# Optimization experiments

Measured on AMD Instinct MI355X. Metric: run time of the kernel, lower is better.

## Reference

```python
import jax, jax.numpy as jnp
import numpy as np

B, T, C = 2, 2048, 1024
H, D = 16, 64  # n_head, head_size = C // H


def setup_inputs() -> dict:
    key = jax.random.key(0)
    ks = jax.random.split(key, 6)
    s = 1.0 / np.sqrt(C)
    x = jax.random.normal(ks[0], (B, T, C), dtype=jnp.float32)
    Wq = jax.random.normal(ks[1], (C, C), dtype=jnp.float32) * s
    Wk = jax.random.normal(ks[2], (C, C), dtype=jnp.float32) * s
    Wv = jax.random.normal(ks[3], (C, C), dtype=jnp.float32) * s
    Wp = jax.random.normal(ks[4], (C, C), dtype=jnp.float32) * s
    bp = jnp.zeros((C,), dtype=jnp.float32)
    return {"x": x, "Wq": Wq, "Wk": Wk, "Wv": Wv, "Wp": Wp, "bp": bp}


def _feature_map(x):
    # F.elu(x) + 1.0
    return jnp.where(x > 0, x + 1.0, jnp.exp(x))


def reference(x, Wq, Wk, Wv, Wp, bp):
    Bx, Tx, Cx = x.shape
    # q,k,v projections (nn.Linear with weight W applies x @ W.T)
    q = (x @ Wq.T).reshape(Bx, Tx, H, D).transpose(0, 2, 1, 3)  # bhtd
    k = (x @ Wk.T).reshape(Bx, Tx, H, D).transpose(0, 2, 1, 3)
    v = (x @ Wv.T).reshape(Bx, Tx, H, D).transpose(0, 2, 1, 3)
    qp = _feature_map(q)
    kp = _feature_map(k)
    # cumulative outer-product context: (B,H,T,D,D)
    kv_cum = jnp.cumsum(jnp.einsum('bhsd,bhsv->bhsdv', kp, v), axis=2)
    ksum_cum = jnp.cumsum(kp, axis=2)  # (B,H,T,D)
    num = jnp.einsum('bhsd,bhsdv->bhsv', qp, kv_cum)
    den = jnp.einsum('bhsd,bhsd->bhs', qp, ksum_cum)[..., None] + 1e-6
    y = (num / den).transpose(0, 2, 1, 3).reshape(Bx, Tx, Cx)
    out = y @ Wp.T + bp  # dropout(p=0) is identity
    new_kv = kv_cum[:, :, -1]
    new_ksum = ksum_cum[:, :, -1]
    return (out, new_kv, new_ksum)
```

## Files before the change

kernel.cpp:

```cpp
#include <hip/hip_runtime.h>
#include <math.h>

#define BB 2
#define TT 2048
#define CC 1024
#define HH 16
#define DD 64
#define MM (BB*TT)
#define LCH 128
#define NCH (TT/LCH)
#define BHH (BB*HH)

#define OUT_OFF_KV   4194304
#define OUT_OFF_KSUM 4325376
#define MB 1048576

typedef unsigned int u32;
typedef unsigned short u16;
typedef __attribute__((ext_vector_type(8))) short s16x8;
typedef __attribute__((ext_vector_type(8))) unsigned short us8;
typedef __attribute__((ext_vector_type(4))) float f32x4;

__device__ __forceinline__ float fmap(float x) {
    return x > 0.0f ? x + 1.0f : expf(x);
}
__device__ __forceinline__ u16 bf16r(float f) {
    u32 u = __float_as_uint(f);
    u += 0x7fffu + ((u >> 16) & 1u);
    return (u16)(u >> 16);
}
__device__ __forceinline__ float bf2f(u16 u) {
    return __uint_as_float(((u32)u) << 16);
}
__device__ __forceinline__ void gload16(const void* g, void* l) {
    __builtin_amdgcn_global_load_lds(
        (const __attribute__((address_space(1))) u32*)g,
        (__attribute__((address_space(3))) u32*)l, 16, 0, 0);
}

__global__ __launch_bounds__(256)
void f2bf_all(const float* __restrict__ x,
              const float* __restrict__ Wq, const float* __restrict__ Wk,
              const float* __restrict__ Wv, const float* __restrict__ Wp,
              u16* __restrict__ xbf, u16* __restrict__ wbf)
{
    const int i = blockIdx.x * 256 + threadIdx.x;
    const float* src;
    u16* dst;
    int off;
    if (i < 524288) {
        src = x; dst = xbf; off = i;
    } else {
        const int j = i - 524288;
        const int sel = j >> 17;
        off = j & 131071;
        src = (sel == 0) ? Wq : (sel == 1) ? Wk : (sel == 2) ? Wv : Wp;
        dst = wbf + ((size_t)sel << 20);
    }
    const float4 a = ((const float4*)src)[off*2];
    const float4 b = ((const float4*)src)[off*2 + 1];
    us8 p;
    p[0]=bf16r(a.x); p[1]=bf16r(a.y); p[2]=bf16r(a.z); p[3]=bf16r(a.w);
    p[4]=bf16r(b.x); p[5]=bf16r(b.y); p[6]=bf16r(b.z); p[7]=bf16r(b.w);
    ((us8*)dst)[off] = p;
}

__global__ __launch_bounds__(512, 4)
void lca_gemm_qkv128(const u16* __restrict__ A, const u16* __restrict__ Wall,
                     u16* __restrict__ qp, u16* __restrict__ kp,
                     u16* __restrict__ kt, u16* __restrict__ vt)
{
    extern __shared__ char LB[];
    const int tid  = threadIdx.x;
    const int lane = tid & 63;
    const int wid  = tid >> 6;
    const int wm   = wid >> 2;
    const int wn   = wid & 3;
    const int bm0  = blockIdx.y * 128;
    const int bn0g = blockIdx.x * 128;
    const int sel  = bn0g >> 10;
    const int nn0  = bn0g & (CC-1);
    const u16* W = Wall + ((size_t)sel << 20);
    const int NT = CC / 64;

    const int srow = (wid << 3) + (lane >> 3);
    const int sg   = lane & 7;
    auto STAGE = [&](const u16* G, int ldsbase) {
        #pragma unroll
        for (int j = 0; j < 2; ++j) {
            const int r  = j*64 + srow;
            const int gs = sg ^ (r & 7);
            gload16(G + (size_t)r * CC + gs*8,
                    LB + ldsbase + (size_t)(j*64 + (wid<<3))*128);
        }
    };
    #define LDSA(slot) ((slot)*16384)
    #define LDSB(slot) (32768 + (slot)*16384)

    f32x4 acc[4][2];
    #pragma unroll
    for (int mi = 0; mi < 4; ++mi)
        #pragma unroll
        for (int ni = 0; ni < 2; ++ni)
            acc[mi][ni] = (f32x4){0.f, 0.f, 0.f, 0.f};

    STAGE(A + (size_t)bm0 * CC + 0, LDSA(0));
    STAGE(W + (size_t)nn0 * CC + 0, LDSB(0));

    const int lr  = lane & 15;
    const int lg4 = lane >> 4;

    for (int t = 0; t < NT; ++t) {
        const int slot = t & 1;

        if (t+1 < NT) {
            STAGE(A + (size_t)bm0 * CC + (t+1)*64, LDSA(slot^1));
            STAGE(W + (size_t)nn0 * CC + (t+1)*64, LDSB(slot^1));
        }
        __builtin_amdgcn_sched_barrier(0);
        if (t < NT-1) asm volatile("s_waitcnt vmcnt(4)" ::: "memory");
        else          asm volatile("s_waitcnt vmcnt(0)" ::: "memory");
        __builtin_amdgcn_s_barrier();

        s16x8 af[4][2], bf[2][2];
        #pragma unroll
        for (int mi = 0; mi < 4; ++mi) {
            const int r = wm*64 + mi*16 + lr;
            #pragma unroll
            for (int ks = 0; ks < 2; ++ks) {
                const int gg = (ks*4 + lg4) ^ (r & 7);
                af[mi][ks] = *(const s16x8*)(LB + LDSA(slot) + r*128 + gg*16);
            }
        }
        #pragma unroll
        for (int ni = 0; ni < 2; ++ni) {
            const int r = wn*32 + ni*16 + lr;
            #pragma unroll
            for (int ks = 0; ks < 2; ++ks) {
                const int gg = (ks*4 + lg4) ^ (r & 7);
                bf[ni][ks] = *(const s16x8*)(LB + LDSB(slot) + r*128 + gg*16);
            }
        }

        __builtin_amdgcn_s_setprio(1);
        #pragma unroll
        for (int mi = 0; mi < 4; ++mi)
            #pragma unroll
            for (int ni = 0; ni < 2; ++ni)
                #pragma unroll
                for (int ks = 0; ks < 2; ++ks)
                    acc[mi][ni] = __builtin_amdgcn_mfma_f32_16x16x32_bf16(
                        af[mi][ks], bf[ni][ks], acc[mi][ni], 0, 0, 0);
        __builtin_amdgcn_s_setprio(0);
        __builtin_amdgcn_sched_barrier(0);
        __builtin_amdgcn_s_barrier();
    }

    #pragma unroll
    for (int mi = 0; mi < 4; ++mi) {
        #pragma unroll
        for (int ni = 0; ni < 2; ++ni) {
            const int coln = nn0 + wn*32 + ni*16 + lr;
            const int rb   = bm0 + wm*64 + mi*16 + lg4*4;
            const int h = coln >> 6, d = coln & (DD-1);
            const int b = rb >> 11, t0 = rb & (TT-1);
            u16 bvv[4];
            #pragma unroll
            for (int r = 0; r < 4; ++r) {
                float val = acc[mi][ni][r];
                if (sel != 2) val = fmap(val);
                bvv[r] = bf16r(val);
            }
            if (sel == 0) {
                u16* p = qp + (((size_t)(b*HH + h)) * TT + t0) * DD + d;
                #pragma unroll
                for (int r = 0; r < 4; ++r) p[(size_t)r * DD] = bvv[r];
            } else {
                const int ch = t0 >> 7, tc = t0 & (LCH-1);
                u16* pt = (sel == 1 ? kt : vt)
                        + (((size_t)((b*HH + h)*NCH + ch)) * DD + d) * LCH + tc;
                *(ushort4*)pt = make_ushort4(bvv[0], bvv[1], bvv[2], bvv[3]);
                if (sel == 1) {
                    u16* p = kp + (((size_t)(b*HH + h)) * TT + t0) * DD + d;
                    #pragma unroll
                    for (int r = 0; r < 4; ++r) p[(size_t)r * DD] = bvv[r];
                }
            }
        }
    }
    #undef LDSA
    #undef LDSB
}

__global__ __launch_bounds__(256)
void lca_gemm_out(const u16* __restrict__ A, const u16* __restrict__ W,
                  const float* __restrict__ bias, float* __restrict__ out)
{
    __shared__ short As[2][4096];
    __shared__ short Bs2[2][2048];
    const int tid  = threadIdx.x;
    const int lane = tid & 63;
    const int wid  = tid >> 6;

    const int bid = blockIdx.y * gridDim.x + blockIdx.x;
    const int nb  = (bid & 7) * 64 + (bid >> 3);
    const int bm0 = (nb >> 4) * 128;
    const int bn0 = (nb & 15) * 64;

    const int wm = wid >> 1, wn = wid & 1;

    const int rsA = wid*32 + (lane >> 2);
    const int rsB = wid*16 + (lane >> 2);
    const int kc  = (lane & 3) * 8;

    f32x4 acc[4][2];
    #pragma unroll
    for (int i = 0; i < 4; ++i)
        #pragma unroll
        for (int j = 0; j < 2; ++j)
            acc[i][j] = (f32x4){0.f, 0.f, 0.f, 0.f};

    const int rA = wm*64 + (lane & 15);
    const int rB = wn*32 + (lane & 15);
    const int kk = (lane >> 4) * 8;

    #pragma unroll
    for (int j = 0; j < 2; ++j)
        gload16(A + (size_t)(bm0 + rsA + j*16) * CC + kc, &As[0][wid*1024 + j*512]);
    gload16(W + (size_t)(bn0 + rsB) * CC + kc, &Bs2[0][wid*512]);
    __syncthreads();

    int cur = 0;
    for (int k0 = 0; k0 < CC; k0 += 32) {
        if (k0 + 32 < CC) {
            #pragma unroll
            for (int j = 0; j < 2; ++j)
                gload16(A + (size_t)(bm0 + rsA + j*16) * CC + k0 + 32 + kc, &As[cur^1][wid*1024 + j*512]);
            gload16(W + (size_t)(bn0 + rsB) * CC + k0 + 32 + kc, &Bs2[cur^1][wid*512]);
        }

        s16x8 af[4], bf[2];
        #pragma unroll
        for (int mi = 0; mi < 4; ++mi) af[mi] = *(const s16x8*)(&As[cur][(rA + mi*16)*32 + kk]);
        #pragma unroll
        for (int ni = 0; ni < 2; ++ni) bf[ni] = *(const s16x8*)(&Bs2[cur][(rB + ni*16)*32 + kk]);
        #pragma unroll
        for (int mi = 0; mi < 4; ++mi)
            #pragma unroll
            for (int ni = 0; ni < 2; ++ni)
                acc[mi][ni] = __builtin_amdgcn_mfma_f32_16x16x32_bf16(af[mi], bf[ni], acc[mi][ni], 0, 0, 0);

        __syncthreads();
        cur ^= 1;
    }

    #pragma unroll
    for (int mi = 0; mi < 4; ++mi) {
        #pragma unroll
        for (int ni = 0; ni < 2; ++ni) {
            const int col = bn0 + wn*32 + ni*16 + (lane & 15);
            const int rb  = bm0 + wm*64 + mi*16 + (lane >> 4)*4;
            const float bb = bias[col];
            #pragma unroll
            for (int r = 0; r < 4; ++r)
                out[(size_t)(rb + r) * CC + col] = acc[mi][ni][r] + bb;
        }
    }
}

__global__ __launch_bounds__(256)
void lca_pass1(const u16* __restrict__ kt, const u16* __restrict__ vt,
               float* __restrict__ Sloc, float* __restrict__ ksloc)
{
    const int wid = threadIdx.x >> 6, lane = threadIdx.x & 63;
    const int c = blockIdx.x * 4 + wid, bh = blockIdx.y;
    const u16* kg = kt + ((size_t)bh * NCH + c) * DD * LCH;
    const u16* vg = vt + ((size_t)bh * NCH + c) * DD * LCH;
    const int lr = lane & 15;
    const int lk = (lane >> 4) * 8;

    f32x4 acc[4][4];
    #pragma unroll
    for (int i = 0; i < 4; ++i)
        #pragma unroll
        for (int j = 0; j < 4; ++j)
            acc[i][j] = (f32x4){0.f, 0.f, 0.f, 0.f};

    #pragma unroll
    for (int ks = 0; ks < 4; ++ks) {
        const int k = ks*32 + lk;
        s16x8 af[4], bf[4];
        #pragma unroll
        for (int mi = 0; mi < 4; ++mi) af[mi] = *(const s16x8*)(kg + (size_t)(mi*16 + lr)*LCH + k);
        #pragma unroll
        for (int ni = 0; ni < 4; ++ni) bf[ni] = *(const s16x8*)(vg + (size_t)(ni*16 + lr)*LCH + k);
        #pragma unroll
        for (int mi = 0; mi < 4; ++mi)
            #pragma unroll
            for (int ni = 0; ni < 4; ++ni)
                acc[mi][ni] = __builtin_amdgcn_mfma_f32_16x16x32_bf16(af[mi], bf[ni], acc[mi][ni], 0, 0, 0);
    }

    float* So = Sloc + ((size_t)bh * NCH + c) * (DD*DD);
    #pragma unroll
    for (int mi = 0; mi < 4; ++mi)
        #pragma unroll
        for (int ni = 0; ni < 4; ++ni) {
            const int e = ni*16 + lr;
            #pragma unroll
            for (int r = 0; r < 4; ++r) {
                const int d = mi*16 + (lane >> 4)*4 + r;
                So[(size_t)d * DD + e] = acc[mi][ni][r];
            }
        }

    float s = 0.0f;
    #pragma unroll
    for (int i = 0; i < 16; ++i) {
        s16x8 dv = *(const s16x8*)(kg + (size_t)lane * LCH + i*8);
        #pragma unroll
        for (int j = 0; j < 8; ++j) s += bf2f((u16)dv[j]);
    }
    ksloc[((size_t)bh * NCH + c) * DD + lane] = s;
}

__global__ __launch_bounds__(256)
void lca_pass2(const float* __restrict__ Sloc, const float* __restrict__ ksloc,
               u16* __restrict__ pst, float* __restrict__ pksx,
               float* __restrict__ out)
{
    const int bh = blockIdx.x;
    const int tid = threadIdx.x;
    const int d0 = (tid >> 4) * 4;
    const int e0 = (tid & 15) * 4;

    float run[4][4] = {};
    for (int c = 0; c < NCH; ++c) {
        u16* P = pst + ((size_t)bh * NCH + c) * (DD*DD);
        #pragma unroll
        for (int i = 0; i < 4; ++i)
            #pragma unroll
            for (int j = 0; j < 4; ++j)
                P[(size_t)(e0 + j) * DD + (d0 + i)] = bf16r(run[i][j]);
        const float* S = Sloc + ((size_t)bh * NCH + c) * (DD*DD);
        #pragma unroll
        for (int i = 0; i < 4; ++i) {
            const float4 t4 = *(const float4*)(S + (size_t)(d0 + i) * DD + e0);
            run[i][0] += t4.x; run[i][1] += t4.y; run[i][2] += t4.z; run[i][3] += t4.w;
        }
    }
    float* nkv = out + OUT_OFF_KV + (size_t)bh * (DD*DD);
    #pragma unroll
    for (int i = 0; i < 4; ++i)
        *(float4*)(nkv + (size_t)(d0 + i) * DD + e0) =
            make_float4(run[i][0], run[i][1], run[i][2], run[i][3]);

    if (tid < DD) {
        float r = 0.0f;
        for (int c = 0; c < NCH; ++c) {
            pksx[((size_t)bh * NCH + c) * DD + tid] = r;
            r += ksloc[((size_t)bh * NCH + c) * DD + tid];
        }
        out[OUT_OFF_KSUM + (size_t)bh * DD + tid] = r;
    }
}

__global__ __launch_bounds__(256)
void lca_pass3(const u16* __restrict__ qp, const u16* __restrict__ kp,
               const u16* __restrict__ vt, const u16* __restrict__ pst,
               const float* __restrict__ pksx, u16* __restrict__ ybf)
{
    __shared__ short SA[16384];
    __shared__ short VS[8192];
    __shared__ short PS[4096];
    __shared__ float pks_s[DD];
    __shared__ float den_s[LCH];

    char* SAb = (char*)SA;
    char* VSb = (char*)VS;
    char* PSb = (char*)PS;

    const int c = blockIdx.x, bh = blockIdx.y;
    const int tid = threadIdx.x;
    const int lane = tid & 63, wid = tid >> 6;

    const u16* qg = qp + ((size_t)bh * TT + (size_t)c * LCH) * DD;
    const u16* kg = kp + ((size_t)bh * TT + (size_t)c * LCH) * DD;
    const u16* vg = vt + ((size_t)bh * NCH + c) * DD * LCH;
    const u16* pg = pst + ((size_t)bh * NCH + c) * (DD*DD);

    for (int i = tid; i < 1024; i += 256) {
        const int row = i >> 3, cc = i & 7;
        const s16x8 dv = *(const s16x8*)(qg + (size_t)row*DD + cc*8);
        *(s16x8*)(SAb + ((row*128 + cc*16) ^ ((row & 7) << 4))) = dv;
    }
    for (int i = tid; i < 1024; i += 256) {
        const int row = i >> 3, cc = i & 7;
        const s16x8 dv = *(const s16x8*)(kg + (size_t)row*DD + cc*8);
        *(s16x8*)(SAb + 16384 + ((row*128 + cc*16) ^ ((row & 7) << 4))) = dv;
    }
    for (int i = tid; i < 1024; i += 256) {
        const int row = i >> 4, cc = i & 15;
        const s16x8 dv = *(const s16x8*)(vg + (size_t)row*LCH + cc*8);
        *(s16x8*)(VSb + ((row*256 + cc*16) ^ ((row & 7) << 4))) = dv;
    }
    for (int i = tid; i < 512; i += 256) {
        const int row = i >> 3, cc = i & 7;
        const s16x8 dv = *(const s16x8*)(pg + (size_t)row*DD + cc*8);
        *(s16x8*)(PSb + ((row*128 + cc*16) ^ ((row & 7) << 4))) = dv;
    }
    if (tid < DD) pks_s[tid] = pksx[((size_t)bh * NCH + c) * DD + tid];
    __syncthreads();

    if (tid < LCH) {
        const int t = tid;
        float s = 1e-6f;
        #pragma unroll
        for (int cc = 0; cc < 8; ++cc) {
            const s16x8 dv = *(const s16x8*)(SAb + ((t*128 + cc*16) ^ ((t & 7) << 4)));
            #pragma unroll
            for (int j = 0; j < 8; ++j) s += bf2f((u16)dv[j]) * pks_s[cc*8 + j];
        }
        den_s[t] = s;
    }

    const int wrow0 = wid * 32;
    const int lr = lane & 15;
    const int lg = lane >> 4;
    const int lk = lg * 8;

    f32x4 sacc[2][8];
    #pragma unroll
    for (int mi = 0; mi < 2; ++mi)
        #pragma unroll
        for (int ni = 0; ni < 8; ++ni)
            sacc[mi][ni] = (f32x4){0.f, 0.f, 0.f, 0.f};

    #pragma unroll
    for (int ks = 0; ks < 2; ++ks) {
        const int k2 = (ks*32 + lk) * 2;
        s16x8 af[2];
        #pragma unroll
        for (int mi = 0; mi < 2; ++mi) {
            const int row = wrow0 + mi*16 + lr;
            af[mi] = *(const s16x8*)(SAb + ((row*128 + k2) ^ ((row & 7) << 4)));
        }
        #pragma unroll
        for (int ni = 0; ni < 8; ++ni) {
            const int rowb = ni*16 + lr;
            const s16x8 bf = *(const s16x8*)(SAb + 16384 + ((rowb*128 + k2) ^ ((rowb & 7) << 4)));
            sacc[0][ni] = __builtin_amdgcn_mfma_f32_16x16x32_bf16(af[0], bf, sacc[0][ni], 0, 0, 0);
            sacc[1][ni] = __builtin_amdgcn_mfma_f32_16x16x32_bf16(af[1], bf, sacc[1][ni], 0, 0, 0);
        }
    }

    f32x4 pv[2][4];
    #pragma unroll
    for (int mi = 0; mi < 2; ++mi)
        #pragma unroll
        for (int ni = 0; ni < 4; ++ni)
            pv[mi][ni] = (f32x4){0.f, 0.f, 0.f, 0.f};

    #pragma unroll
    for (int ks = 0; ks < 2; ++ks) {
        const int k2 = (ks*32 + lk) * 2;
        s16x8 af[2];
        #pragma unroll
        for (int mi = 0; mi < 2; ++mi) {
            const int row = wrow0 + mi*16 + lr;
            af[mi] = *(const s16x8*)(SAb + ((row*128 + k2) ^ ((row & 7) << 4)));
        }
        #pragma unroll
        for (int ni = 0; ni < 4; ++ni) {
            const int rowb = ni*16 + lr;
            const s16x8 bf = *(const s16x8*)(PSb + ((rowb*128 + k2) ^ ((rowb & 7) << 4)));
            pv[0][ni] = __builtin_amdgcn_mfma_f32_16x16x32_bf16(af[0], bf, pv[0][ni], 0, 0, 0);
            pv[1][ni] = __builtin_amdgcn_mfma_f32_16x16x32_bf16(af[1], bf, pv[1][ni], 0, 0, 0);
        }
    }
    __syncthreads();

    #pragma unroll
    for (int mi = 0; mi < 2; ++mi) {
        float dr[4] = {0.f, 0.f, 0.f, 0.f};
        #pragma unroll
        for (int ni = 0; ni < 8; ++ni) {
            const int tp = ni*16 + lr;
            #pragma unroll
            for (int r = 0; r < 4; ++r) {
                const int t = wrow0 + mi*16 + lg*4 + r;
                const float v = (tp <= t) ? sacc[mi][ni][r] : 0.f;
                dr[r] += v;
                *(u16*)(SAb + ((t*256 + tp*2) ^ ((t & 7) << 4))) = bf16r(v);
            }
        }
        #pragma unroll
        for (int r = 0; r < 4; ++r) {
            float s = dr[r];
            s += __shfl_xor(s, 1); s += __shfl_xor(s, 2);
            s += __shfl_xor(s, 4); s += __shfl_xor(s, 8);
            if (lr == 0) {
                const int t = wrow0 + mi*16 + lg*4 + r;
                den_s[t] += s;
            }
        }
    }
    __syncthreads();

    #pragma unroll
    for (int ks = 0; ks < 4; ++ks) {
        const int k2 = (ks*32 + lk) * 2;
        s16x8 af[2];
        #pragma unroll
        for (int mi = 0; mi < 2; ++mi) {
            const int row = wrow0 + mi*16 + lr;
            af[mi] = *(const s16x8*)(SAb + ((row*256 + k2) ^ ((row & 7) << 4)));
        }
        #pragma unroll
        for (int ni = 0; ni < 4; ++ni) {
            const int rowb = ni*16 + lr;
            const s16x8 bf = *(const s16x8*)(VSb + ((rowb*256 + k2) ^ ((rowb & 7) << 4)));
            pv[0][ni] = __builtin_amdgcn_mfma_f32_16x16x32_bf16(af[0], bf, pv[0][ni], 0, 0, 0);
            pv[1][ni] = __builtin_amdgcn_mfma_f32_16x16x32_bf16(af[1], bf, pv[1][ni], 0, 0, 0);
        }
    }

    const int b = bh >> 4, h = bh & (HH-1);
    #pragma unroll
    for (int mi = 0; mi < 2; ++mi)
        #pragma unroll
        for (int ni = 0; ni < 4; ++ni) {
            const int e = ni*16 + lr;
            #pragma unroll
            for (int r = 0; r < 4; ++r) {
                const int t = wrow0 + mi*16 + lg*4 + r;
                const float y = pv[mi][ni][r] / den_s[t];
                ybf[((size_t)(b*TT) + (size_t)c*LCH + t) * CC + h*DD + e] = bf16r(y);
            }
        }
}

extern "C" void kernel_launch(void* const* d_in, const int* in_sizes, int n_in,
                              void* d_out, int out_size, void* d_ws, size_t ws_size,
                              hipStream_t stream) {
    const float* x  = (const float*)d_in[0];
    const float* Wq = (const float*)d_in[1];
    const float* Wk = (const float*)d_in[2];
    const float* Wv = (const float*)d_in[3];
    const float* Wp = (const float*)d_in[4];
    const float* bp = (const float*)d_in[5];
    float* out = (float*)d_out;
    char* ws = (char*)d_ws;

    u16*   xbf  = (u16*)(ws + 0);
    u16*   Wbf  = (u16*)(ws + (size_t)8*MB);
    u16*   qp   = (u16*)(ws + (size_t)16*MB);
    u16*   kp   = (u16*)(ws + (size_t)24*MB);
    u16*   kt   = (u16*)(ws + (size_t)32*MB);
    u16*   vt   = (u16*)(ws + (size_t)40*MB);
    u16*   ybf  = (u16*)(ws + (size_t)48*MB);
    float* Sl   = (float*)(ws + (size_t)56*MB);
    float* ksl  = (float*)(ws + (size_t)64*MB);
    float* pksx = (float*)(ws + (size_t)64*MB + 131072);
    u16*   pst  = (u16*)(ws + (size_t)65*MB);

    (void)hipFuncSetAttribute((const void*)lca_gemm_qkv128,
                              hipFuncAttributeMaxDynamicSharedMemorySize, 65536);

    f2bf_all<<<4096, 256, 0, stream>>>(x, Wq, Wk, Wv, Wp, xbf, Wbf);

    lca_gemm_qkv128<<<dim3(3*CC/128, MM/128), 512, 65536, stream>>>(xbf, Wbf, qp, kp, kt, vt);

    lca_pass1<<<dim3(NCH/4, BHH), 256, 0, stream>>>(kt, vt, Sl, ksl);
    lca_pass2<<<BHH, 256, 0, stream>>>(Sl, ksl, pst, pksx, out);
    lca_pass3<<<dim3(NCH, BHH), 256, 0, stream>>>(qp, kp, vt, pst, pksx, ybf);

    lca_gemm_out<<<dim3(CC/64, MM/128), 256, 0, stream>>>(ybf, Wbf + ((size_t)3 << 20), bp, out);
}
```

Measured before the change: 116.9 us.

## Restructure output GEMM with K=64 tiles, XOR-swizzled LDS and vmcnt pipelining

```diff
diff --git a/kernel.cpp b/kernel.cpp
--- a/kernel.cpp
+++ b/kernel.cpp
@@ -192,80 +192,116 @@
     #undef LDSB
 }
 
-__global__ __launch_bounds__(256)
+__global__ __launch_bounds__(256, 3)
 void lca_gemm_out(const u16* __restrict__ A, const u16* __restrict__ W,
                   const float* __restrict__ bias, float* __restrict__ out)
 {
-    __shared__ short As[2][4096];
-    __shared__ short Bs2[2][2048];
+    extern __shared__ char LB[];
     const int tid  = threadIdx.x;
     const int lane = tid & 63;
     const int wid  = tid >> 6;
-
-    const int bid = blockIdx.y * gridDim.x + blockIdx.x;
-    const int nb  = (bid & 7) * 64 + (bid >> 3);
-    const int bm0 = (nb >> 4) * 128;
-    const int bn0 = (nb & 15) * 64;
-
-    const int wm = wid >> 1, wn = wid & 1;
-
-    const int rsA = wid*32 + (lane >> 2);
-    const int rsB = wid*16 + (lane >> 2);
-    const int kc  = (lane & 3) * 8;
+    const int wm   = wid >> 1;
+    const int wn   = wid & 1;
+    const int bm0  = blockIdx.y * 128;
+    const int bn0  = blockIdx.x * 64;
+    const int NT = CC / 64;
+
+    const int srw = tid >> 3;
+    const int sg  = tid & 7;
+    auto STAGE_A = [&](const u16* G, int ldsbase) {
+        #pragma unroll
+        for (int j = 0; j < 4; ++j) {
+            const int r  = j*32 + srw;
+            const int gs = sg ^ (r & 7);
+            gload16(G + (size_t)r * CC + gs*8,
+                    LB + ldsbase + (size_t)j*4096 + (size_t)tid*16);
+        }
+    };
+    auto STAGE_B = [&](const u16* G, int ldsbase) {
+        #pragma unroll
+        for (int j = 0; j < 2; ++j) {
+            const int r  = j*32 + srw;
+            const int gs = sg ^ (r & 7);
+            gload16(G + (size_t)r * CC + gs*8,
+                    LB + ldsbase + (size_t)j*4096 + (size_t)tid*16);
+        }
+    };
+    #define LDSA(slot) ((slot)*16384)
+    #define LDSB(slot) (32768 + (slot)*8192)
 
     f32x4 acc[4][2];
     #pragma unroll
-    for (int i = 0; i < 4; ++i)
-        #pragma unroll
-        for (int j = 0; j < 2; ++j)
-            acc[i][j] = (f32x4){0.f, 0.f, 0.f, 0.f};
-
-    const int rA = wm*64 + (lane & 15);
-    const int rB = wn*32 + (lane & 15);
-    const int kk = (lane >> 4) * 8;
-
-    #pragma unroll
-    for (int j = 0; j < 2; ++j)
-        gload16(A + (size_t)(bm0 + rsA + j*16) * CC + kc, &As[0][wid*1024 + j*512]);
-    gload16(W + (size_t)(bn0 + rsB) * CC + kc, &Bs2[0][wid*512]);
-    __syncthreads();
-
-    int cur = 0;
-    for (int k0 = 0; k0 < CC; k0 += 32) {
-        if (k0 + 32 < CC) {
-            #pragma unroll
-            for (int j = 0; j < 2; ++j)
-                gload16(A + (size_t)(bm0 + rsA + j*16) * CC + k0 + 32 + kc, &As[cur^1][wid*1024 + j*512]);
-            gload16(W + (size_t)(bn0 + rsB) * CC + k0 + 32 + kc, &Bs2[cur^1][wid*512]);
-        }
-
-        s16x8 af[4], bf[2];
-        #pragma unroll
-        for (int mi = 0; mi < 4; ++mi) af[mi] = *(const s16x8*)(&As[cur][(rA + mi*16)*32 + kk]);
-        #pragma unroll
-        for (int ni = 0; ni < 2; ++ni) bf[ni] = *(const s16x8*)(&Bs2[cur][(rB + ni*16)*32 + kk]);
+    for (int mi = 0; mi < 4; ++mi)
+        #pragma unroll
+        for (int ni = 0; ni < 2; ++ni)
+            acc[mi][ni] = (f32x4){0.f, 0.f, 0.f, 0.f};
+
+    STAGE_A(A + (size_t)bm0 * CC + 0, LDSA(0));
+    STAGE_B(W + (size_t)bn0 * CC + 0, LDSB(0));
+
+    const int lr  = lane & 15;
+    const int lg4 = lane >> 4;
+
+    for (int t = 0; t < NT; ++t) {
+        const int slot = t & 1;
+
+        if (t+1 < NT) {
+            STAGE_A(A + (size_t)bm0 * CC + (t+1)*64, LDSA(slot^1));
+            STAGE_B(W + (size_t)bn0 * CC + (t+1)*64, LDSB(slot^1));
+        }
+        __builtin_amdgcn_sched_barrier(0);
+        if (t < NT-1) asm volatile("s_waitcnt vmcnt(6)" ::: "memory");
+        else          asm volatile("s_waitcnt vmcnt(0)" ::: "memory");
+        __builtin_amdgcn_s_barrier();
+
+        s16x8 af[4][2], bf[2][2];
+        #pragma unroll
+        for (int mi = 0; mi < 4; ++mi) {
+            const int r = wm*64 + mi*16 + lr;
+            #pragma unroll
+            for (int ks = 0; ks < 2; ++ks) {
+                const int gg = (ks*4 + lg4) ^ (r & 7);
+                af[mi][ks] = *(const s16x8*)(LB + LDSA(slot) + r*128 + gg*16);
+            }
+        }
+        #pragma unroll
+        for (int ni = 0; ni < 2; ++ni) {
+            const int r = wn*32 + ni*16 + lr;
+            #pragma unroll
+            for (int ks = 0; ks < 2; ++ks) {
+                const int gg = (ks*4 + lg4) ^ (r & 7);
+                bf[ni][ks] = *(const s16x8*)(LB + LDSB(slot) + r*128 + gg*16);
+            }
+        }
+
+        __builtin_amdgcn_s_setprio(1);
         #pragma unroll
         for (int mi = 0; mi < 4; ++mi)
             #pragma unroll
             for (int ni = 0; ni < 2; ++ni)
-                acc[mi][ni] = __builtin_amdgcn_mfma_f32_16x16x32_bf16(af[mi], bf[ni], acc[mi][ni], 0, 0, 0);
-
-        __syncthreads();
-        cur ^= 1;
+                #pragma unroll
+                for (int ks = 0; ks < 2; ++ks)
+                    acc[mi][ni] = __builtin_amdgcn_mfma_f32_16x16x32_bf16(
+                        af[mi][ks], bf[ni][ks], acc[mi][ni], 0, 0, 0);
+        __builtin_amdgcn_s_setprio(0);
+        __builtin_amdgcn_sched_barrier(0);
+        __builtin_amdgcn_s_barrier();
     }
 
     #pragma unroll
     for (int mi = 0; mi < 4; ++mi) {
         #pragma unroll
         for (int ni = 0; ni < 2; ++ni) {
-            const int col = bn0 + wn*32 + ni*16 + (lane & 15);
-            const int rb  = bm0 + wm*64 + mi*16 + (lane >> 4)*4;
+            const int col = bn0 + wn*32 + ni*16 + lr;
+            const int rb  = bm0 + wm*64 + mi*16 + lg4*4;
             const float bb = bias[col];
             #pragma unroll
             for (int r = 0; r < 4; ++r)
                 out[(size_t)(rb + r) * CC + col] = acc[mi][ni][r] + bb;
         }
     }
+    #undef LDSA
+    #undef LDSB
 }
 
 __global__ __launch_bounds__(256)
@@ -566,6 +602,8 @@
 
     (void)hipFuncSetAttribute((const void*)lca_gemm_qkv128,
                               hipFuncAttributeMaxDynamicSharedMemorySize, 65536);
+    (void)hipFuncSetAttribute((const void*)lca_gemm_out,
+                              hipFuncAttributeMaxDynamicSharedMemorySize, 49152);
 
     f2bf_all<<<4096, 256, 0, stream>>>(x, Wq, Wk, Wv, Wp, xbf, Wbf);
 
@@ -575,5 +613,5 @@
     lca_pass2<<<BHH, 256, 0, stream>>>(Sl, ksl, pst, pksx, out);
     lca_pass3<<<dim3(NCH, BHH), 256, 0, stream>>>(qp, kp, vt, pst, pksx, ybf);
 
-    lca_gemm_out<<<dim3(CC/64, MM/128), 256, 0, stream>>>(ybf, Wbf + ((size_t)3 << 20), bp, out);
-}
+    lca_gemm_out<<<dim3(CC/64, MM/128), 256, 49152, stream>>>(ybf, Wbf + ((size_t)3 << 20), bp, out);
+}
```

Result: faster. 108.7 us (-7.0%).
